# Performance work log

Hardware: AMD Instinct MI355X
Metric: run time of the kernel (lower is better)

## Reference

```python
import math
import jax, jax.numpy as jnp
from jax import lax
import numpy as np

E = 16        # num experts
K = 2         # top_k
CF = 1.25     # capacity factor


def setup_inputs() -> dict:
    key = jax.random.key(0)
    k0, k1, k2, k3, k4 = jax.random.split(key, 5)
    B, S, D, H = 2, 2048, 1024, 1024
    scale = 0.02
    return {
        "x": jax.random.normal(k0, (B, S, D), dtype=jnp.float32),
        "router_w": jax.random.normal(k1, (D, E), dtype=jnp.float32) * scale,
        "gate_w": jax.random.normal(k2, (E, D, H), dtype=jnp.float32) * scale,
        "up_w": jax.random.normal(k3, (E, D, H), dtype=jnp.float32) * scale,
        "down_w": jax.random.normal(k4, (E, H, D), dtype=jnp.float32) * scale,
    }


def reference(x, router_w, gate_w, up_w, down_w):
    B, S, D = x.shape
    xf = x.reshape(-1, D)                     # [T, D]
    T = B * S
    capacity = max(1, math.ceil(T * K / E * CF))   # static python int
    Cbuf = K * capacity                       # per-expert buffer (per-column capacity x K)

    # ---- router: softmax over experts, then top-k (weights = top-k probs) ----
    logits = xf @ router_w                    # [T, E]
    probs = jax.nn.softmax(logits, axis=-1)
    w, idx = lax.top_k(probs, K)              # [T, K] each

    # ---- capacity drop: per k-column, per expert, keep first `capacity` tokens ----
    oh = jax.nn.one_hot(idx, E, dtype=w.dtype)            # [T, K, E]
    rank = jnp.cumsum(oh, axis=0) - oh                     # exclusive rank per (k, e)
    myrank = jnp.sum(rank * oh, axis=-1)                   # [T, K]
    keep = myrank < capacity
    w = jnp.where(keep, w, 0.0)

    # ---- dispatch: scatter kept assignments into [E, Cbuf] slots ----
    flat_e = idx.reshape(-1)                               # [A], A = T*K (row-major: token-major)
    flat_w = w.reshape(-1)
    keep_f = keep.reshape(-1)
    tok = jnp.repeat(jnp.arange(T, dtype=jnp.int32), K)    # [A]
    ohk = jax.nn.one_hot(flat_e, E, dtype=jnp.int32) * keep_f[:, None].astype(jnp.int32)
    pos = jnp.cumsum(ohk, axis=0) - ohk                    # exclusive rank among kept per expert
    slot = jnp.sum(pos * ohk, axis=-1)                     # [A], < Cbuf for kept
    e_idx = jnp.where(keep_f, flat_e, E)                   # dropped -> dummy expert row E

    dispatch = jnp.full((E + 1, Cbuf), T, dtype=jnp.int32).at[e_idx, slot].set(tok)
    wbuf = jnp.zeros((E + 1, Cbuf), dtype=w.dtype).at[e_idx, slot].set(flat_w)
    dispatch = dispatch[:E]
    wbuf = wbuf[:E]

    x_pad = jnp.concatenate([xf, jnp.zeros((1, D), xf.dtype)], axis=0)  # sentinel row
    xe = x_pad[dispatch]                                   # [E, Cbuf, D]

    # ---- grouped SwiGLU expert GEMMs ----
    gate = jnp.einsum('ecd,edh->ech', xe, gate_w)
    up = jnp.einsum('ecd,edh->ech', xe, up_w)
    hidden = jax.nn.silu(gate) * up
    out = jnp.einsum('ech,ehd->ecd', hidden, down_w)       # [E, Cbuf, D]
    out = out * wbuf[:, :, None]

    # ---- combine: scatter-add back to tokens ----
    combined = jnp.zeros((T + 1, D), dtype=xf.dtype).at[dispatch.reshape(-1)].add(out.reshape(-1, D))
    return combined[:T].reshape(B, S, D)
```

## Files before the change

### kernel.cpp

```cpp
#include <hip/hip_runtime.h>
#include <math.h>

#define T_TOK 4096
#define DIM   1024
#define HID   1024
#define NE    16
#define CAP   640
#define CBUF  1280
#define BM 128
#define BN 128
#define BK 32
#define MAXTILE 160

typedef __attribute__((ext_vector_type(8))) short short8;
typedef __attribute__((ext_vector_type(4))) float f32x4;

static __device__ __forceinline__ unsigned short f2bf(float f) {
    unsigned int u = __float_as_uint(f);
    u += 0x7fff + ((u >> 16) & 1);
    return (unsigned short)(u >> 16);
}

static __device__ __forceinline__ void async16(const void* g, void* l) {
    __builtin_amdgcn_global_load_lds((const __attribute__((address_space(1))) void*)g,
                                     (__attribute__((address_space(3))) void*)l, 16, 0, 0);
}

__global__ void convert_x_k(const float* __restrict__ x, unsigned short* __restrict__ xb) {
    int i = blockIdx.x * blockDim.x + threadIdx.x;
    int base = i * 4;
    int row = base >> 10;
    ushort4 o;
    if (row < T_TOK) {
        float4 v = *(const float4*)(x + base);
        o.x = f2bf(v.x); o.y = f2bf(v.y); o.z = f2bf(v.z); o.w = f2bf(v.w);
    } else {
        o.x = 0; o.y = 0; o.z = 0; o.w = 0;
    }
    *(ushort4*)(xb + base) = o;
}

#define TSP 68
__global__ void transpose_cvt_k(const float* __restrict__ W0, const float* __restrict__ W1,
                                const float* __restrict__ W2,
                                unsigned short* __restrict__ T0, unsigned short* __restrict__ T1,
                                unsigned short* __restrict__ T2) {
    __shared__ unsigned short s[64 * TSP];
    int zz = blockIdx.z;
    int which = zz >> 4, e = zz & 15;
    const float* W = (which == 0) ? W0 : (which == 1) ? W1 : W2;
    unsigned short* T = (which == 0) ? T0 : (which == 1) ? T1 : T2;
    const float* Wp = W + (size_t)e * DIM * HID;
    unsigned short* Tp = T + (size_t)e * DIM * HID;
    int k0 = blockIdx.y * 64, n0 = blockIdx.x * 64;
    int tid = threadIdx.x;
    int tx = tid & 15, ty = tid >> 4;
    #pragma unroll
    for (int i = 0; i < 4; ++i) {
        int k = ty + i * 16;
        float4 v = *(const float4*)(Wp + (size_t)(k0 + k) * 1024 + n0 + tx * 4);
        int nb = tx * 4;
        s[(nb + 0) * TSP + k] = f2bf(v.x);
        s[(nb + 1) * TSP + k] = f2bf(v.y);
        s[(nb + 2) * TSP + k] = f2bf(v.z);
        s[(nb + 3) * TSP + k] = f2bf(v.w);
    }
    __syncthreads();
    int n = tid >> 2, cseg = (tid & 3) * 16;
    union { ushort4 h[4]; uint4 q[2]; } u;
    #pragma unroll
    for (int j = 0; j < 4; ++j)
        u.h[j] = *(ushort4*)&s[n * TSP + cseg + 4 * j];
    unsigned short* orow = Tp + (size_t)(n0 + n) * 1024 + k0 + cseg;
    *(uint4*)(orow + 0) = u.q[0];
    *(uint4*)(orow + 8) = u.q[1];
}

__global__ void router_k(const float* __restrict__ x, const float* __restrict__ rw,
                         int* __restrict__ route_e, float* __restrict__ route_w) {
    int t = blockIdx.x;
    int lane = threadIdx.x;
    const float* xr = x + (size_t)t * DIM + lane * 16;
    float4 xv0 = *(const float4*)(xr + 0);
    float4 xv1 = *(const float4*)(xr + 4);
    float4 xv2 = *(const float4*)(xr + 8);
    float4 xv3 = *(const float4*)(xr + 12);
    float xl[16] = {xv0.x, xv0.y, xv0.z, xv0.w, xv1.x, xv1.y, xv1.z, xv1.w,
                    xv2.x, xv2.y, xv2.z, xv2.w, xv3.x, xv3.y, xv3.z, xv3.w};
    float p[16];
    #pragma unroll
    for (int e = 0; e < 16; ++e) p[e] = 0.f;
    #pragma unroll
    for (int j = 0; j < 16; ++j) {
        const float4* rp = (const float4*)(rw + (size_t)(lane * 16 + j) * 16);
        float4 r0 = rp[0], r1 = rp[1], r2 = rp[2], r3 = rp[3];
        float xv = xl[j];
        p[0]  += xv * r0.x; p[1]  += xv * r0.y; p[2]  += xv * r0.z; p[3]  += xv * r0.w;
        p[4]  += xv * r1.x; p[5]  += xv * r1.y; p[6]  += xv * r1.z; p[7]  += xv * r1.w;
        p[8]  += xv * r2.x; p[9]  += xv * r2.y; p[10] += xv * r2.z; p[11] += xv * r2.w;
        p[12] += xv * r3.x; p[13] += xv * r3.y; p[14] += xv * r3.z; p[15] += xv * r3.w;
    }
    #pragma unroll
    for (int off = 32; off > 0; off >>= 1) {
        #pragma unroll
        for (int e = 0; e < 16; ++e) p[e] += __shfl_xor(p[e], off);
    }
    if (lane == 0) {
        float m = p[0];
        #pragma unroll
        for (int e = 1; e < 16; ++e) m = fmaxf(m, p[e]);
        float s = 0.f;
        #pragma unroll
        for (int e = 0; e < 16; ++e) s = s + __expf(p[e] - m);
        float v0 = -1e30f, v1 = -1e30f; int i0 = 0, i1 = 0;
        #pragma unroll
        for (int e = 0; e < 16; ++e) {
            float v = p[e];
            if (v > v0)      { v1 = v0; i1 = i0; v0 = v; i0 = e; }
            else if (v > v1) { v1 = v;  i1 = e; }
        }
        route_e[t*2+0] = i0;  route_e[t*2+1] = i1;
        route_w[t*2+0] = __expf(v0 - m) / s;
        route_w[t*2+1] = __expf(v1 - m) / s;
    }
}

__global__ __launch_bounds__(1024)
void build_dispatch_k(const int* __restrict__ route_e, const float* __restrict__ route_w,
                      int* __restrict__ disp, float* __restrict__ wbuf, int* __restrict__ tmeta) {
    __shared__ unsigned char eidx[2 * T_TOK];
    __shared__ unsigned char keepf[2 * T_TOK];
    __shared__ int totals[NE];
    int tid = threadIdx.x;
    int wv = tid >> 6, lane = tid & 63;

    {
        int4 a = ((const int4*)route_e)[tid * 2];
        int4 b = ((const int4*)route_e)[tid * 2 + 1];
        unsigned int lo = (a.x & 0xff) | ((a.y & 0xff) << 8) | ((a.z & 0xff) << 16) | ((a.w & 0xff) << 24);
        unsigned int hi = (b.x & 0xff) | ((b.y & 0xff) << 8) | ((b.z & 0xff) << 16) | ((b.w & 0xff) << 24);
        uint2 pk; pk.x = lo; pk.y = hi;
        *(uint2*)(eidx + tid * 8) = pk;
    }
    __syncthreads();

    unsigned long long below = (lane == 0) ? 0ull : ((~0ull) >> (64 - lane));
    #pragma unroll
    for (int s = 0; s < 2; ++s) {
        int st = wv + s * 16;
        int e = st >> 1, k = st & 1;
        int run = 0;
        for (int base = 0; base < T_TOK; base += 64) {
            int t = base + lane;
            int hit = (eidx[t * 2 + k] == e);
            unsigned long long m = __ballot(hit);
            int rank = run + __popcll(m & below);
            if (hit) keepf[t * 2 + k] = (rank < CAP) ? 1 : 0;
            run += __popcll(m);
        }
    }
    __syncthreads();

    {
        int e = wv;
        int run = 0;
        for (int base = 0; base < 2 * T_TOK; base += 64) {
            int f = base + lane;
            int hit = (eidx[f] == e) && keepf[f];
            unsigned long long m = __ballot(hit);
            int slot = run + __popcll(m & below);
            if (hit) {
                disp[e * CBUF + slot] = f >> 1;
                wbuf[e * CBUF + slot] = route_w[f];
            }
            run += __popcll(m);
        }
        if (lane == 0) totals[e] = run;
    }
    __syncthreads();

    for (int i = tid; i < NE * CBUF; i += 1024) {
        int e = i / CBUF, s = i - e * CBUF;
        if (s >= totals[e]) { disp[i] = T_TOK; wbuf[i] = 0.f; }
    }

    if (tid == 0) {
        int n = 0;
        for (int e = 0; e < NE; ++e) {
            int ntl = (totals[e] + BM - 1) / BM;
            for (int m = 0; m < ntl; ++m) { tmeta[4 + n] = (e << 8) | m; ++n; }
        }
        tmeta[0] = n;
    }
}

__global__ __launch_bounds__(256, 2)
void gemm1_k(const unsigned short* __restrict__ xb, const unsigned short* __restrict__ gt,
             const unsigned short* __restrict__ ut, const int* __restrict__ disp,
             const int* __restrict__ tmeta, unsigned short* __restrict__ hidden) {
    int slot = blockIdx.y;
    if (slot >= tmeta[0]) return;
    int pk = tmeta[4 + slot];
    int e = pk >> 8, mt = pk & 255;
    int m0 = mt * BM, n0 = blockIdx.x * BN;

    __shared__ unsigned short As[BM * BK];
    __shared__ unsigned short Bg[BN * BK];
    __shared__ unsigned short Bu[BN * BK];
    __shared__ int tok[BM];
    int tid = threadIdx.x;
    if (tid < BM) tok[tid] = disp[e * CBUF + m0 + tid];
    __syncthreads();

    int lane = tid & 63, w = tid >> 6;
    int cg = (lane & 3) ^ ((lane >> 3) & 3);
    int rl = lane >> 2;
    int rA0 = w * 32 + rl, rA1 = rA0 + 16;
    const unsigned short* srcA0 = xb + (size_t)tok[rA0] * DIM + cg * 8;
    const unsigned short* srcA1 = xb + (size_t)tok[rA1] * DIM + cg * 8;
    const unsigned short* srcG0 = gt + ((size_t)e * HID + n0 + rA0) * DIM + cg * 8;
    const unsigned short* srcG1 = gt + ((size_t)e * HID + n0 + rA1) * DIM + cg * 8;
    const unsigned short* srcU0 = ut + ((size_t)e * HID + n0 + rA0) * DIM + cg * 8;
    const unsigned short* srcU1 = ut + ((size_t)e * HID + n0 + rA1) * DIM + cg * 8;
    unsigned short* dA0 = As + (size_t)(w * 32) * BK;
    unsigned short* dA1 = As + (size_t)(w * 32 + 16) * BK;
    unsigned short* dG0 = Bg + (size_t)(w * 32) * BK;
    unsigned short* dG1 = Bg + (size_t)(w * 32 + 16) * BK;
    unsigned short* dU0 = Bu + (size_t)(w * 32) * BK;
    unsigned short* dU1 = Bu + (size_t)(w * 32 + 16) * BK;

    int wm = w >> 1, wn = w & 1;
    int quad = lane >> 4, ln = lane & 15;
    int swq = quad ^ ((ln >> 1) & 3);

    f32x4 zero4 = {0.f, 0.f, 0.f, 0.f};
    f32x4 accg[4][4], accu[4][4];
    #pragma unroll
    for (int i = 0; i < 4; ++i)
        #pragma unroll
        for (int j = 0; j < 4; ++j) { accg[i][j] = zero4; accu[i][j] = zero4; }

    for (int k0 = 0; k0 < DIM; k0 += BK) {
        async16(srcA0, dA0); async16(srcA1, dA1);
        async16(srcG0, dG0); async16(srcG1, dG1);
        async16(srcU0, dU0); async16(srcU1, dU1);
        srcA0 += BK; srcA1 += BK; srcG0 += BK; srcG1 += BK; srcU0 += BK; srcU1 += BK;
        asm volatile("s_waitcnt vmcnt(0)" ::: "memory");
        __syncthreads();
        short8 af[4], bgf[4], buf2[4];
        #pragma unroll
        for (int i = 0; i < 4; ++i)
            af[i] = *(const short8*)(As + (wm * 64 + i * 16 + ln) * BK + swq * 8);
        #pragma unroll
        for (int j = 0; j < 4; ++j) {
            bgf[j]  = *(const short8*)(Bg + (wn * 64 + j * 16 + ln) * BK + swq * 8);
            buf2[j] = *(const short8*)(Bu + (wn * 64 + j * 16 + ln) * BK + swq * 8);
        }
        #pragma unroll
        for (int i = 0; i < 4; ++i)
            #pragma unroll
            for (int j = 0; j < 4; ++j) {
                accg[i][j] = __builtin_amdgcn_mfma_f32_16x16x32_bf16(af[i], bgf[j],  accg[i][j], 0, 0, 0);
                accu[i][j] = __builtin_amdgcn_mfma_f32_16x16x32_bf16(af[i], buf2[j], accu[i][j], 0, 0, 0);
            }
        __syncthreads();
    }
    #pragma unroll
    for (int i = 0; i < 4; ++i) {
        #pragma unroll
        for (int r = 0; r < 4; ++r) {
            int row = m0 + wm * 64 + i * 16 + quad * 4 + r;
            unsigned short* hrow = hidden + ((size_t)e * CBUF + row) * HID + n0 + wn * 64 + ln;
            #pragma unroll
            for (int j = 0; j < 4; ++j) {
                float g = accg[i][j][r];
                float u = accu[i][j][r];
                float sg = g / (1.f + __expf(-g));
                hrow[j * 16] = f2bf(sg * u);
            }
        }
    }
}

__global__ __launch_bounds__(256, 2)
void gemm2_k(const unsigned short* __restrict__ hidden, const unsigned short* __restrict__ dt,
             const int* __restrict__ disp, const float* __restrict__ wb,
             const int* __restrict__ tmeta, float* __restrict__ out) {
    int slot = blockIdx.y;
    if (slot >= tmeta[0]) return;
    int pk = tmeta[4 + slot];
    int e = pk >> 8, mt = pk & 255;
    int m0 = mt * BM, n0 = blockIdx.x * BN;

    __shared__ unsigned short As[BM * BK];
    __shared__ unsigned short Bs[BN * BK];
    __shared__ int tok[BM];
    __shared__ float twf[BM];
    int tid = threadIdx.x;
    if (tid < BM) {
        tok[tid] = disp[e * CBUF + m0 + tid];
        twf[tid] = wb[e * CBUF + m0 + tid];
    }
    __syncthreads();

    int lane = tid & 63, w = tid >> 6;
    int cg = (lane & 3) ^ ((lane >> 3) & 3);
    int rl = lane >> 2;
    int rA0 = w * 32 + rl, rA1 = rA0 + 16;
    const unsigned short* srcA0 = hidden + ((size_t)e * CBUF + m0 + rA0) * HID + cg * 8;
    const unsigned short* srcA1 = hidden + ((size_t)e * CBUF + m0 + rA1) * HID + cg * 8;
    const unsigned short* srcB0 = dt + ((size_t)e * DIM + n0 + rA0) * HID + cg * 8;
    const unsigned short* srcB1 = dt + ((size_t)e * DIM + n0 + rA1) * HID + cg * 8;
    unsigned short* dA0 = As + (size_t)(w * 32) * BK;
    unsigned short* dA1 = As + (size_t)(w * 32 + 16) * BK;
    unsigned short* dB0 = Bs + (size_t)(w * 32) * BK;
    unsigned short* dB1 = Bs + (size_t)(w * 32 + 16) * BK;

    int wm = w >> 1, wn = w & 1;
    int quad = lane >> 4, ln = lane & 15;
    int swq = quad ^ ((ln >> 1) & 3);

    f32x4 zero4 = {0.f, 0.f, 0.f, 0.f};
    f32x4 acc[4][4];
    #pragma unroll
    for (int i = 0; i < 4; ++i)
        #pragma unroll
        for (int j = 0; j < 4; ++j) acc[i][j] = zero4;

    for (int k0 = 0; k0 < HID; k0 += BK) {
        async16(srcA0, dA0); async16(srcA1, dA1);
        async16(srcB0, dB0); async16(srcB1, dB1);
        srcA0 += BK; srcA1 += BK; srcB0 += BK; srcB1 += BK;
        asm volatile("s_waitcnt vmcnt(0)" ::: "memory");
        __syncthreads();
        short8 af[4], bf[4];
        #pragma unroll
        for (int i = 0; i < 4; ++i)
            af[i] = *(const short8*)(As + (wm * 64 + i * 16 + ln) * BK + swq * 8);
        #pragma unroll
        for (int j = 0; j < 4; ++j)
            bf[j] = *(const short8*)(Bs + (wn * 64 + j * 16 + ln) * BK + swq * 8);
        #pragma unroll
        for (int i = 0; i < 4; ++i)
            #pragma unroll
            for (int j = 0; j < 4; ++j)
                acc[i][j] = __builtin_amdgcn_mfma_f32_16x16x32_bf16(af[i], bf[j], acc[i][j], 0, 0, 0);
        __syncthreads();
    }
    #pragma unroll
    for (int i = 0; i < 4; ++i) {
        #pragma unroll
        for (int r = 0; r < 4; ++r) {
            int rl2 = wm * 64 + i * 16 + quad * 4 + r;
            int t = tok[rl2];
            float wgt = twf[rl2];
            if (t < T_TOK) {
                float* orow = out + (size_t)t * DIM + n0 + wn * 64 + ln;
                #pragma unroll
                for (int j = 0; j < 4; ++j)
                    atomicAdd(&orow[j * 16], acc[i][j][r] * wgt);
            }
        }
    }
}

extern "C" void kernel_launch(void* const* d_in, const int* in_sizes, int n_in,
                              void* d_out, int out_size, void* d_ws, size_t ws_size,
                              hipStream_t stream) {
    const float* x  = (const float*)d_in[0];
    const float* rw = (const float*)d_in[1];
    const float* gw = (const float*)d_in[2];
    const float* uw = (const float*)d_in[3];
    const float* dw = (const float*)d_in[4];
    float* out = (float*)d_out;

    char* ws = (char*)d_ws;
    size_t off = 0;
    auto alloc = [&](size_t bytes) { void* p = ws + off; off += (bytes + 255) & ~(size_t)255; return p; };
    unsigned short* xb  = (unsigned short*)alloc((size_t)(T_TOK + 1) * DIM * 2);
    unsigned short* gt  = (unsigned short*)alloc((size_t)NE * DIM * HID * 2);
    unsigned short* ut  = (unsigned short*)alloc((size_t)NE * DIM * HID * 2);
    unsigned short* dtw = (unsigned short*)alloc((size_t)NE * DIM * HID * 2);
    unsigned short* hid = (unsigned short*)alloc((size_t)NE * CBUF * HID * 2);
    int*   disp   = (int*)alloc((size_t)NE * CBUF * 4);
    float* wbf    = (float*)alloc((size_t)NE * CBUF * 4);
    int*   tmeta  = (int*)alloc((4 + MAXTILE) * 4);
    int*   re     = (int*)alloc((size_t)T_TOK * 2 * 4);
    float* rwt    = (float*)alloc((size_t)T_TOK * 2 * 4);
    (void)ws_size; (void)in_sizes; (void)n_in;

    hipMemsetAsync(d_out, 0, (size_t)out_size * sizeof(float), stream);
    convert_x_k<<<T_TOK + 1, 256, 0, stream>>>(x, xb);
    transpose_cvt_k<<<dim3(16, 16, 48), 256, 0, stream>>>(gw, uw, dw, gt, ut, dtw);
    router_k<<<T_TOK, 64, 0, stream>>>(x, rw, re, rwt);
    build_dispatch_k<<<1, 1024, 0, stream>>>(re, rwt, disp, wbf, tmeta);
    gemm1_k<<<dim3(HID / BN, MAXTILE), 256, 0, stream>>>(xb, gt, ut, disp, tmeta, hid);
    gemm2_k<<<dim3(DIM / BN, MAXTILE), 256, 0, stream>>>(hid, dtw, disp, wbf, tmeta, out);
}
```

Before: 444.9 us.

## Double-buffer expert GEMM LDS tiles and replace atomic combine with gather kernel

Both expert GEMMs now double-buffer their LDS tiles, prefetching the next K slice while MFMAs run on the current one, with a single barrier per iteration. The second GEMM no longer scatters weighted float atomics into the output. It writes bf16 per-slot results into a buffer that reuses the gate-weight workspace, and a new combine kernel gathers each token's two slots through a slot map and applies the routing weights. This removes the output memset and the atomic contention, at the cost of an extra bf16 round trip of the expert outputs and an additional kernel launch.

```diff
diff --git a/kernel.cpp b/kernel.cpp
--- a/kernel.cpp
+++ b/kernel.cpp
@@ -127,7 +127,7 @@
 
 __global__ __launch_bounds__(1024)
 void build_dispatch_k(const int* __restrict__ route_e, const float* __restrict__ route_w,
-                      int* __restrict__ disp, float* __restrict__ wbuf, int* __restrict__ tmeta) {
+                      int* __restrict__ disp, int* __restrict__ smap, int* __restrict__ tmeta) {
     __shared__ unsigned char eidx[2 * T_TOK];
     __shared__ unsigned char keepf[2 * T_TOK];
     __shared__ int totals[NE];
@@ -142,6 +142,7 @@
         uint2 pk; pk.x = lo; pk.y = hi;
         *(uint2*)(eidx + tid * 8) = pk;
     }
+    for (int i = tid; i < 2 * T_TOK; i += 1024) smap[i] = -1;
     __syncthreads();
 
     unsigned long long below = (lane == 0) ? 0ull : ((~0ull) >> (64 - lane));
@@ -171,7 +172,7 @@
             int slot = run + __popcll(m & below);
             if (hit) {
                 disp[e * CBUF + slot] = f >> 1;
-                wbuf[e * CBUF + slot] = route_w[f];
+                smap[f] = e * CBUF + slot;
             }
             run += __popcll(m);
         }
@@ -181,7 +182,7 @@
 
     for (int i = tid; i < NE * CBUF; i += 1024) {
         int e = i / CBUF, s = i - e * CBUF;
-        if (s >= totals[e]) { disp[i] = T_TOK; wbuf[i] = 0.f; }
+        if (s >= totals[e]) disp[i] = T_TOK;
     }
 
     if (tid == 0) {
@@ -204,9 +205,9 @@
     int e = pk >> 8, mt = pk & 255;
     int m0 = mt * BM, n0 = blockIdx.x * BN;
 
-    __shared__ unsigned short As[BM * BK];
-    __shared__ unsigned short Bg[BN * BK];
-    __shared__ unsigned short Bu[BN * BK];
+    __shared__ unsigned short As[2 * BM * BK];
+    __shared__ unsigned short Bg[2 * BN * BK];
+    __shared__ unsigned short Bu[2 * BN * BK];
     __shared__ int tok[BM];
     int tid = threadIdx.x;
     if (tid < BM) tok[tid] = disp[e * CBUF + m0 + tid];
@@ -222,12 +223,12 @@
     const unsigned short* srcG1 = gt + ((size_t)e * HID + n0 + rA1) * DIM + cg * 8;
     const unsigned short* srcU0 = ut + ((size_t)e * HID + n0 + rA0) * DIM + cg * 8;
     const unsigned short* srcU1 = ut + ((size_t)e * HID + n0 + rA1) * DIM + cg * 8;
-    unsigned short* dA0 = As + (size_t)(w * 32) * BK;
-    unsigned short* dA1 = As + (size_t)(w * 32 + 16) * BK;
-    unsigned short* dG0 = Bg + (size_t)(w * 32) * BK;
-    unsigned short* dG1 = Bg + (size_t)(w * 32 + 16) * BK;
-    unsigned short* dU0 = Bu + (size_t)(w * 32) * BK;
-    unsigned short* dU1 = Bu + (size_t)(w * 32 + 16) * BK;
+    unsigned short* dA0 = As + (w * 32) * BK;
+    unsigned short* dA1 = As + (w * 32 + 16) * BK;
+    unsigned short* dG0 = Bg + (w * 32) * BK;
+    unsigned short* dG1 = Bg + (w * 32 + 16) * BK;
+    unsigned short* dU0 = Bu + (w * 32) * BK;
+    unsigned short* dU1 = Bu + (w * 32 + 16) * BK;
 
     int wm = w >> 1, wn = w & 1;
     int quad = lane >> 4, ln = lane & 15;
@@ -240,21 +241,33 @@
         #pragma unroll
         for (int j = 0; j < 4; ++j) { accg[i][j] = zero4; accu[i][j] = zero4; }
 
+    async16(srcA0, dA0); async16(srcA1, dA1);
+    async16(srcG0, dG0); async16(srcG1, dG1);
+    async16(srcU0, dU0); async16(srcU1, dU1);
+
     for (int k0 = 0; k0 < DIM; k0 += BK) {
-        async16(srcA0, dA0); async16(srcA1, dA1);
-        async16(srcG0, dG0); async16(srcG1, dG1);
-        async16(srcU0, dU0); async16(srcU1, dU1);
-        srcA0 += BK; srcA1 += BK; srcG0 += BK; srcG1 += BK; srcU0 += BK; srcU1 += BK;
-        asm volatile("s_waitcnt vmcnt(0)" ::: "memory");
-        __syncthreads();
+        int cur = (k0 >> 5) & 1;
+        asm volatile("s_waitcnt vmcnt(0)\n\ts_barrier" ::: "memory");
+        if (k0 + BK < DIM) {
+            int nx = cur ^ 1, nk = k0 + BK;
+            async16(srcA0 + nk, dA0 + nx * (BM * BK));
+            async16(srcA1 + nk, dA1 + nx * (BM * BK));
+            async16(srcG0 + nk, dG0 + nx * (BN * BK));
+            async16(srcG1 + nk, dG1 + nx * (BN * BK));
+            async16(srcU0 + nk, dU0 + nx * (BN * BK));
+            async16(srcU1 + nk, dU1 + nx * (BN * BK));
+        }
+        const unsigned short* Ab = As + cur * (BM * BK);
+        const unsigned short* Gb = Bg + cur * (BN * BK);
+        const unsigned short* Ub = Bu + cur * (BN * BK);
         short8 af[4], bgf[4], buf2[4];
         #pragma unroll
         for (int i = 0; i < 4; ++i)
-            af[i] = *(const short8*)(As + (wm * 64 + i * 16 + ln) * BK + swq * 8);
+            af[i] = *(const short8*)(Ab + (wm * 64 + i * 16 + ln) * BK + swq * 8);
         #pragma unroll
         for (int j = 0; j < 4; ++j) {
-            bgf[j]  = *(const short8*)(Bg + (wn * 64 + j * 16 + ln) * BK + swq * 8);
-            buf2[j] = *(const short8*)(Bu + (wn * 64 + j * 16 + ln) * BK + swq * 8);
+            bgf[j]  = *(const short8*)(Gb + (wn * 64 + j * 16 + ln) * BK + swq * 8);
+            buf2[j] = *(const short8*)(Ub + (wn * 64 + j * 16 + ln) * BK + swq * 8);
         }
         #pragma unroll
         for (int i = 0; i < 4; ++i)
@@ -263,7 +276,6 @@
                 accg[i][j] = __builtin_amdgcn_mfma_f32_16x16x32_bf16(af[i], bgf[j],  accg[i][j], 0, 0, 0);
                 accu[i][j] = __builtin_amdgcn_mfma_f32_16x16x32_bf16(af[i], buf2[j], accu[i][j], 0, 0, 0);
             }
-        __syncthreads();
     }
     #pragma unroll
     for (int i = 0; i < 4; ++i) {
@@ -284,24 +296,16 @@
 
 __global__ __launch_bounds__(256, 2)
 void gemm2_k(const unsigned short* __restrict__ hidden, const unsigned short* __restrict__ dt,
-             const int* __restrict__ disp, const float* __restrict__ wb,
-             const int* __restrict__ tmeta, float* __restrict__ out) {
+             const int* __restrict__ tmeta, unsigned short* __restrict__ ebuf) {
     int slot = blockIdx.y;
     if (slot >= tmeta[0]) return;
     int pk = tmeta[4 + slot];
     int e = pk >> 8, mt = pk & 255;
     int m0 = mt * BM, n0 = blockIdx.x * BN;
 
-    __shared__ unsigned short As[BM * BK];
-    __shared__ unsigned short Bs[BN * BK];
-    __shared__ int tok[BM];
-    __shared__ float twf[BM];
+    __shared__ unsigned short As[2 * BM * BK];
+    __shared__ unsigned short Bs[2 * BN * BK];
     int tid = threadIdx.x;
-    if (tid < BM) {
-        tok[tid] = disp[e * CBUF + m0 + tid];
-        twf[tid] = wb[e * CBUF + m0 + tid];
-    }
-    __syncthreads();
 
     int lane = tid & 63, w = tid >> 6;
     int cg = (lane & 3) ^ ((lane >> 3) & 3);
@@ -311,10 +315,10 @@
     const unsigned short* srcA1 = hidden + ((size_t)e * CBUF + m0 + rA1) * HID + cg * 8;
     const unsigned short* srcB0 = dt + ((size_t)e * DIM + n0 + rA0) * HID + cg * 8;
     const unsigned short* srcB1 = dt + ((size_t)e * DIM + n0 + rA1) * HID + cg * 8;
-    unsigned short* dA0 = As + (size_t)(w * 32) * BK;
-    unsigned short* dA1 = As + (size_t)(w * 32 + 16) * BK;
-    unsigned short* dB0 = Bs + (size_t)(w * 32) * BK;
-    unsigned short* dB1 = Bs + (size_t)(w * 32 + 16) * BK;
+    unsigned short* dA0 = As + (w * 32) * BK;
+    unsigned short* dA1 = As + (w * 32 + 16) * BK;
+    unsigned short* dB0 = Bs + (w * 32) * BK;
+    unsigned short* dB1 = Bs + (w * 32 + 16) * BK;
 
     int wm = w >> 1, wn = w & 1;
     int quad = lane >> 4, ln = lane & 15;
@@ -327,41 +331,74 @@
         #pragma unroll
         for (int j = 0; j < 4; ++j) acc[i][j] = zero4;
 
+    async16(srcA0, dA0); async16(srcA1, dA1);
+    async16(srcB0, dB0); async16(srcB1, dB1);
+
     for (int k0 = 0; k0 < HID; k0 += BK) {
-        async16(srcA0, dA0); async16(srcA1, dA1);
-        async16(srcB0, dB0); async16(srcB1, dB1);
-        srcA0 += BK; srcA1 += BK; srcB0 += BK; srcB1 += BK;
-        asm volatile("s_waitcnt vmcnt(0)" ::: "memory");
-        __syncthreads();
+        int cur = (k0 >> 5) & 1;
+        asm volatile("s_waitcnt vmcnt(0)\n\ts_barrier" ::: "memory");
+        if (k0 + BK < HID) {
+            int nx = cur ^ 1, nk = k0 + BK;
+            async16(srcA0 + nk, dA0 + nx * (BM * BK));
+            async16(srcA1 + nk, dA1 + nx * (BM * BK));
+            async16(srcB0 + nk, dB0 + nx * (BN * BK));
+            async16(srcB1 + nk, dB1 + nx * (BN * BK));
+        }
+        const unsigned short* Ab = As + cur * (BM * BK);
+        const unsigned short* Bb = Bs + cur * (BN * BK);
         short8 af[4], bf[4];
         #pragma unroll
         for (int i = 0; i < 4; ++i)
-            af[i] = *(const short8*)(As + (wm * 64 + i * 16 + ln) * BK + swq * 8);
+            af[i] = *(const short8*)(Ab + (wm * 64 + i * 16 + ln) * BK + swq * 8);
         #pragma unroll
         for (int j = 0; j < 4; ++j)
-            bf[j] = *(const short8*)(Bs + (wn * 64 + j * 16 + ln) * BK + swq * 8);
+            bf[j] = *(const short8*)(Bb + (wn * 64 + j * 16 + ln) * BK + swq * 8);
         #pragma unroll
         for (int i = 0; i < 4; ++i)
             #pragma unroll
             for (int j = 0; j < 4; ++j)
                 acc[i][j] = __builtin_amdgcn_mfma_f32_16x16x32_bf16(af[i], bf[j], acc[i][j], 0, 0, 0);
-        __syncthreads();
     }
     #pragma unroll
     for (int i = 0; i < 4; ++i) {
         #pragma unroll
         for (int r = 0; r < 4; ++r) {
-            int rl2 = wm * 64 + i * 16 + quad * 4 + r;
-            int t = tok[rl2];
-            float wgt = twf[rl2];
-            if (t < T_TOK) {
-                float* orow = out + (size_t)t * DIM + n0 + wn * 64 + ln;
-                #pragma unroll
-                for (int j = 0; j < 4; ++j)
-                    atomicAdd(&orow[j * 16], acc[i][j][r] * wgt);
+            int row = m0 + wm * 64 + i * 16 + quad * 4 + r;
+            unsigned short* erow = ebuf + ((size_t)e * CBUF + row) * DIM + n0 + wn * 64 + ln;
+            #pragma unroll
+            for (int j = 0; j < 4; ++j)
+                erow[j * 16] = f2bf(acc[i][j][r]);
+        }
+    }
+}
+
+__global__ __launch_bounds__(256)
+void combine_k(const unsigned short* __restrict__ ebuf, const int* __restrict__ smap,
+               const float* __restrict__ rwt, float* __restrict__ out) {
+    int t = blockIdx.x * 2 + (threadIdx.x >> 7);
+    int c = (threadIdx.x & 127) * 8;
+    float acc[8];
+    #pragma unroll
+    for (int j = 0; j < 8; ++j) acc[j] = 0.f;
+    #pragma unroll
+    for (int k = 0; k < 2; ++k) {
+        int sm = smap[t * 2 + k];
+        if (sm >= 0) {
+            float wgt = rwt[t * 2 + k];
+            uint4 rv = *(const uint4*)(ebuf + (size_t)sm * DIM + c);
+            unsigned int d[4] = {rv.x, rv.y, rv.z, rv.w};
+            #pragma unroll
+            for (int q = 0; q < 4; ++q) {
+                acc[q * 2 + 0] += wgt * __uint_as_float(d[q] << 16);
+                acc[q * 2 + 1] += wgt * __uint_as_float(d[q] & 0xffff0000u);
             }
         }
     }
+    float4 o0 = {acc[0], acc[1], acc[2], acc[3]};
+    float4 o1 = {acc[4], acc[5], acc[6], acc[7]};
+    float* orow = out + (size_t)t * DIM + c;
+    *(float4*)(orow + 0) = o0;
+    *(float4*)(orow + 4) = o1;
 }
 
 extern "C" void kernel_launch(void* const* d_in, const int* in_sizes, int n_in,
@@ -383,17 +420,18 @@
     unsigned short* dtw = (unsigned short*)alloc((size_t)NE * DIM * HID * 2);
     unsigned short* hid = (unsigned short*)alloc((size_t)NE * CBUF * HID * 2);
     int*   disp   = (int*)alloc((size_t)NE * CBUF * 4);
-    float* wbf    = (float*)alloc((size_t)NE * CBUF * 4);
+    int*   smap   = (int*)alloc((size_t)T_TOK * 2 * 4);
     int*   tmeta  = (int*)alloc((4 + MAXTILE) * 4);
     int*   re     = (int*)alloc((size_t)T_TOK * 2 * 4);
     float* rwt    = (float*)alloc((size_t)T_TOK * 2 * 4);
+    unsigned short* ebuf = gt;
     (void)ws_size; (void)in_sizes; (void)n_in;
 
-    hipMemsetAsync(d_out, 0, (size_t)out_size * sizeof(float), stream);
     convert_x_k<<<T_TOK + 1, 256, 0, stream>>>(x, xb);
     transpose_cvt_k<<<dim3(16, 16, 48), 256, 0, stream>>>(gw, uw, dw, gt, ut, dtw);
     router_k<<<T_TOK, 64, 0, stream>>>(x, rw, re, rwt);
-    build_dispatch_k<<<1, 1024, 0, stream>>>(re, rwt, disp, wbf, tmeta);
+    build_dispatch_k<<<1, 1024, 0, stream>>>(re, rwt, disp, smap, tmeta);
     gemm1_k<<<dim3(HID / BN, MAXTILE), 256, 0, stream>>>(xb, gt, ut, disp, tmeta, hid);
-    gemm2_k<<<dim3(DIM / BN, MAXTILE), 256, 0, stream>>>(hid, dtw, disp, wbf, tmeta, out);
-}
+    gemm2_k<<<dim3(DIM / BN, MAXTILE), 256, 0, stream>>>(hid, dtw, tmeta, ebuf);
+    combine_k<<<T_TOK / 2, 256, 0, stream>>>(ebuf, smap, rwt, out);
+}
```

Measured after the change: 413.1 us. 1.08x faster.
